# Performance work log

Hardware: AMD Instinct MI355X
Metric: run time of the kernel (lower is better)

## Reference

```python
import jax, jax.numpy as jnp
import numpy as np

B, D, H, W = 8, 256, 128, 128
NCLS, K = 6, 8
RATIO = 0.05
P = int(H * W * RATIO)  # 819 sampled pixels, unique (replace=False in original)


def setup_inputs() -> dict:
    key = jax.random.key(0)
    ks = jax.random.split(key, 6)
    rng = np.random.default_rng(0)
    flat_idx = rng.choice(H * W, P, replace=False)
    return {
        "assp_features": jax.random.normal(ks[0], (B, D, H, W), jnp.float32),
        "prototypes": jax.random.normal(ks[1], (B, NCLS, K, D), jnp.float32),
        "Wk": jax.random.normal(ks[2], (128, D), jnp.float32) * 0.05,
        "bk": jax.random.normal(ks[3], (128,), jnp.float32) * 0.05,
        "Wq": jax.random.normal(ks[4], (NCLS, 128, D), jnp.float32) * 0.05,
        "bq": jax.random.normal(ks[5], (NCLS, 128), jnp.float32) * 0.05,
        "x_coords": jnp.asarray(flat_idx // H, jnp.int32),
        "y_coords": jnp.asarray(flat_idx % H, jnp.int32),
    }


def reference(assp_features, prototypes, Wk, bk, Wq, bq, x_coords, y_coords):
    # DomainTrain branch: detach, then replace sampled pixels with nearest prototype
    feats = jax.lax.stop_gradient(assp_features)                 # [B,D,H,W]
    pf = prototypes.reshape(B, NCLS * K, D)                      # [B,6K,D]
    sel = feats[:, :, x_coords, y_coords].transpose(0, 2, 1)     # [B,P,D]
    # squared distance (||f||^2 constant dropped; argmin unchanged)
    d2 = jnp.sum(pf * pf, -1)[:, None, :] - 2.0 * jnp.einsum('bpd,bcd->bpc', sel, pf)
    idx = jnp.argmin(d2, axis=-1)                                # [B,P]
    newv = jnp.take_along_axis(pf, idx[:, :, None], axis=1)      # [B,P,D]
    feats = feats.at[:, :, x_coords, y_coords].set(newv.transpose(0, 2, 1))

    # key: 1x1 conv -> [B,128,H,W]
    key_out = jnp.einsum('od,bdhw->bohw', Wk, feats) + bk[None, :, None, None]
    # per-class query 1x1 conv applied to each prototype vector -> [B,6,K,128]
    q = jnp.einsum('iod,bijd->bijo', Wq, prototypes) + bq[None, :, None, :]
    # similarity per (class, cluster): [B,6K,H,W], ordering i-major j-minor as in the loop
    sim = jnp.einsum('bijo,bohw->bijhw', q, key_out).reshape(B, NCLS * K, H, W)
    C = NCLS * K
    w = jax.nn.softmax(sim / C * K, axis=1)
    w_max = jnp.max(w, axis=1)                                   # [B,H,W]
    w_mean = jnp.mean(w, axis=1)
    assp_weighted = feats * w_max[:, None]                       # [B,D,H,W]
    prototypes_out = q.reshape(B, NCLS * K, 128).transpose(1, 0, 2)  # list -> stacked [6K,B,128]
    return assp_weighted, prototypes_out, w_max, sim, w_mean
```

## Files before the change

### kernel.cpp

```cpp
#include <hip/hip_runtime.h>

#define B_   8
#define D_   256
#define HW_  16384
#define NC_  48
#define KO_  128
#define PT_  32

using bf16x8 = __attribute__((ext_vector_type(8))) short;
using f32x4  = __attribute__((ext_vector_type(4))) float;
typedef unsigned long long ull;

__device__ __forceinline__ unsigned short f2bf(float f) {
  unsigned int u = __float_as_uint(f);
  u += 0x7FFFu + ((u >> 16) & 1u);
  return (unsigned short)(u >> 16);
}
__device__ __forceinline__ ull pack4bf(float a, float b, float c, float d) {
  return (ull)f2bf(a) | ((ull)f2bf(b) << 16)
       | ((ull)f2bf(c) << 32) | ((ull)f2bf(d) << 48);
}

__global__ __launch_bounds__(128) void p1_kernel(
    const float* __restrict__ protos, const float* __restrict__ Wq,
    const float* __restrict__ bq, const float* __restrict__ Wk,
    const float* __restrict__ bk,
    unsigned short* __restrict__ m_pk, float* __restrict__ beta,
    float* __restrict__ protos_out, int* __restrict__ map_i) {
  __shared__ float qs[KO_];
  const int c = blockIdx.x;
  const int b = blockIdx.y;
  const int o = threadIdx.x;
  const int i = c >> 3;
  const float* wq = Wq + ((size_t)i * KO_ + o) * D_;
  const float* pp = protos + ((size_t)b * NC_ + c) * D_;
  float acc = bq[i * KO_ + o];
  for (int d = 0; d < D_; d += 4) {
    float4 wv = *(const float4*)(wq + d);
    float4 pv = *(const float4*)(pp + d);
    acc += wv.x * pv.x + wv.y * pv.y + wv.z * pv.z + wv.w * pv.w;
  }
  qs[o] = acc;
  protos_out[((size_t)c * B_ + b) * KO_ + o] = acc;
  const int gid = (b * NC_ + c) * KO_ + o;
  if (gid < B_ * HW_ / 4) map_i[gid] = -1;
  __syncthreads();
  float m0 = 0.f, m1 = 0.f;
  for (int oo = 0; oo < KO_; ++oo) {
    float2 wv = *(const float2*)(Wk + (size_t)oo * D_ + o * 2);
    float qv = qs[oo];
    m0 += qv * wv.x;
    m1 += qv * wv.y;
  }
  {
    const int ks = o >> 4, g = (o >> 2) & 3, ii = (o & 3) * 2;
    const int ct = c >> 4, lr = c & 15;
    const size_t fidx = ((size_t)(b * 24 + ks * 3 + ct) * 64 + g * 16 + lr) * 8 + ii;
    unsigned pk = (unsigned)f2bf(m0) | ((unsigned)f2bf(m1) << 16);
    *(unsigned*)(m_pk + fidx) = pk;
  }
  if (o < 64) {
    float p = qs[o] * bk[o] + qs[o + 64] * bk[o + 64];
    for (int off = 32; off; off >>= 1) p += __shfl_down(p, off);
    if (o == 0) beta[b * NC_ + c] = p;
  }
}

__global__ void p2_kernel(const float* __restrict__ feats,
                          const float* __restrict__ protos,
                          const int* __restrict__ xc,
                          const int* __restrict__ yc,
                          signed char* __restrict__ map) {
  const int sp = blockIdx.x;
  const int b  = blockIdx.y;
  const int lane = threadIdx.x;
  __shared__ float sel[D_];
  const int pix = xc[sp] * 128 + yc[sp];
  const float* fb = feats + (size_t)b * D_ * HW_ + pix;
  for (int k = 0; k < 4; ++k) {
    int d = lane + k * 64;
    sel[d] = fb[(size_t)d * HW_];
  }
  __syncthreads();
  float d2 = 3.4e38f;
  int bi = lane;
  if (lane < NC_) {
    const float* pf = protos + ((size_t)b * NC_ + lane) * D_;
    float nrm = 0.f, dot = 0.f;
    for (int d = 0; d < D_; d += 4) {
      float4 pv = *(const float4*)(pf + d);
      float4 sv = *(const float4*)(sel + d);
      nrm += pv.x * pv.x + pv.y * pv.y + pv.z * pv.z + pv.w * pv.w;
      dot += pv.x * sv.x + pv.y * sv.y + pv.z * sv.z + pv.w * sv.w;
    }
    d2 = nrm - 2.f * dot;
  }
  for (int off = 32; off > 0; off >>= 1) {
    float ov = __shfl_down(d2, off);
    int   oi = __shfl_down(bi, off);
    if (ov < d2 || (ov == d2 && oi < bi)) { d2 = ov; bi = oi; }
  }
  if (lane == 0) map[(size_t)b * HW_ + pix] = (signed char)bi;
}

__global__ __launch_bounds__(128, 2) void m_kernel(
    const float* __restrict__ feats, const float* __restrict__ protos,
    const unsigned short* __restrict__ m_pk, const float* __restrict__ beta,
    const signed char* __restrict__ map,
    float* __restrict__ out_assp, float* __restrict__ out_wmax,
    float* __restrict__ out_sim, float* __restrict__ out_wmean) {
  __shared__ __align__(16) unsigned short Fb[PT_ * 256];
  __shared__ __align__(16) float simb[NC_ * PT_];
  __shared__ float wm[PT_];
  __shared__ signed char map_s[PT_];

  const int tid  = threadIdx.x;
  const int lane = tid & 63;
  const int wid  = tid >> 6;
  const int g    = lane >> 4;
  const int lr   = lane & 15;
  const int b    = blockIdx.y;
  const int p0   = blockIdx.x * PT_;

  if (tid < PT_) map_s[tid] = map[(size_t)b * HW_ + p0 + tid];
  __syncthreads();

  unsigned char* fbB = (unsigned char*)Fb;
  const int x  = tid & 7;
  const int dr = tid >> 3;

  float V[64];
  {
    const float* fb = feats + (size_t)b * D_ * HW_ + p0 + x * 4;
    const float* prb = protos + (size_t)b * NC_ * D_;
    int cj[4];
    #pragma unroll
    for (int j = 0; j < 4; ++j) cj[j] = map_s[x * 4 + j];
    #pragma unroll
    for (int it = 0; it < 4; ++it) {
      const int d0 = it * 64 + dr * 4;
      #pragma unroll
      for (int k = 0; k < 4; ++k) {
        float4 t = *(const float4*)(fb + (size_t)(d0 + k) * HW_);
        V[it*16 + k*4 + 0] = t.x; V[it*16 + k*4 + 1] = t.y;
        V[it*16 + k*4 + 2] = t.z; V[it*16 + k*4 + 3] = t.w;
      }
      #pragma unroll
      for (int j = 0; j < 4; ++j) {
        if (cj[j] >= 0) {
          float4 pv = *(const float4*)(prb + (size_t)cj[j] * D_ + d0);
          V[it*16 + 0*4 + j] = pv.x; V[it*16 + 1*4 + j] = pv.y;
          V[it*16 + 2*4 + j] = pv.z; V[it*16 + 3*4 + j] = pv.w;
        }
      }
      #pragma unroll
      for (int j = 0; j < 4; ++j) {
        const int p = x * 4 + j;
        const unsigned X = (unsigned)(((p & 7) << 4) ^ ((p >> 3) << 3));
        *(ull*)(fbB + p * 512 + ((unsigned)(d0 * 2) ^ X)) =
            pack4bf(V[it*16 + 0*4 + j], V[it*16 + 1*4 + j],
                    V[it*16 + 2*4 + j], V[it*16 + 3*4 + j]);
      }
    }
  }
  __syncthreads();

  const int p = wid * 16 + lr;
  const unsigned Xp = (unsigned)(((p & 7) << 4) ^ ((p >> 3) << 3));
  f32x4 sacc[3] = {};
  {
    const unsigned short* apk = m_pk + (size_t)b * 24 * 64 * 8 + lane * 8;
    #pragma unroll
    for (int ks = 0; ks < 8; ++ks) {
      const unsigned base = (unsigned)(ks * 64 + g * 16);
      ull lo = *(const ull*)(fbB + p * 512 + (base ^ Xp));
      ull hi = *(const ull*)(fbB + p * 512 + ((base + 8) ^ Xp));
      union { ull u[2]; bf16x8 v8; } bu;
      bu.u[0] = lo; bu.u[1] = hi;
      #pragma unroll
      for (int ct = 0; ct < 3; ++ct) {
        bf16x8 af = *(const bf16x8*)(apk + (size_t)(ks * 3 + ct) * 64 * 8);
        sacc[ct] = __builtin_amdgcn_mfma_f32_16x16x32_bf16(af, bu.v8, sacc[ct], 0, 0, 0);
      }
    }
  }

  #pragma unroll
  for (int ct = 0; ct < 3; ++ct) {
    float4 bt = *(const float4*)(beta + b * NC_ + ct * 16 + g * 4);
    sacc[ct][0] += bt.x; sacc[ct][1] += bt.y;
    sacc[ct][2] += bt.z; sacc[ct][3] += bt.w;
  }
  float m = -3.4e38f;
  #pragma unroll
  for (int ct = 0; ct < 3; ++ct)
    #pragma unroll
    for (int r = 0; r < 4; ++r) m = fmaxf(m, sacc[ct][r]);
  m = fmaxf(m, __shfl_xor(m, 16));
  m = fmaxf(m, __shfl_xor(m, 32));
  const float sc = 1.0f / 6.0f;
  float s = 0.f;
  #pragma unroll
  for (int ct = 0; ct < 3; ++ct)
    #pragma unroll
    for (int r = 0; r < 4; ++r) s += __expf((sacc[ct][r] - m) * sc);
  s += __shfl_xor(s, 16);
  s += __shfl_xor(s, 32);
  const float wmax = 1.f / s;

  #pragma unroll
  for (int ct = 0; ct < 3; ++ct)
    #pragma unroll
    for (int r = 0; r < 4; ++r)
      simb[(ct * 16 + g * 4 + r) * PT_ + p] = sacc[ct][r];
  const size_t pixg = (size_t)p0 + p;
  if (g == 0) {
    wm[p] = wmax;
    out_wmax[(size_t)b * HW_ + pixg] = wmax;
    out_wmean[(size_t)b * HW_ + pixg] = 1.f / 48.f;
  }
  __syncthreads();

  #pragma unroll
  for (int r3 = 0; r3 < 3; ++r3) {
    const int f  = r3 * 128 + tid;
    const int c  = f >> 3;
    const int po = (f & 7) * 4;
    float4 sv = *(const float4*)(simb + c * PT_ + po);
    *(float4*)(out_sim + ((size_t)b * NC_ + c) * HW_ + p0 + po) = sv;
  }

  {
    float4 w4 = *(const float4*)(wm + x * 4);
    float* oa = out_assp + (size_t)b * D_ * HW_ + p0 + x * 4;
    #pragma unroll
    for (int it = 0; it < 4; ++it) {
      const int d0 = it * 64 + dr * 4;
      #pragma unroll
      for (int k = 0; k < 4; ++k) {
        float4 o;
        o.x = V[it*16 + k*4 + 0] * w4.x;
        o.y = V[it*16 + k*4 + 1] * w4.y;
        o.z = V[it*16 + k*4 + 2] * w4.z;
        o.w = V[it*16 + k*4 + 3] * w4.w;
        *(float4*)(oa + (size_t)(d0 + k) * HW_) = o;
      }
    }
  }
}

extern "C" void kernel_launch(void* const* d_in, const int* in_sizes, int n_in,
                              void* d_out, int out_size, void* d_ws, size_t ws_size,
                              hipStream_t stream) {
  const float* feats  = (const float*)d_in[0];
  const float* protos = (const float*)d_in[1];
  const float* Wk     = (const float*)d_in[2];
  const float* bk     = (const float*)d_in[3];
  const float* Wq     = (const float*)d_in[4];
  const float* bq     = (const float*)d_in[5];
  const int*   xc     = (const int*)d_in[6];
  const int*   yc     = (const int*)d_in[7];
  const int    P      = in_sizes[6];

  float* out       = (float*)d_out;
  float* out_assp  = out;
  float* out_po    = out_assp + (size_t)B_ * D_ * HW_;
  float* out_wmax  = out_po + (size_t)NC_ * B_ * KO_;
  float* out_sim   = out_wmax + (size_t)B_ * HW_;
  float* out_wmean = out_sim + (size_t)B_ * NC_ * HW_;

  unsigned char* ws = (unsigned char*)d_ws;
  unsigned short* m_pk = (unsigned short*)ws;
  float* beta          = (float*)(ws + 196608);
  signed char* map     = (signed char*)(ws + 198144);

  p1_kernel<<<dim3(NC_, B_), 128, 0, stream>>>(protos, Wq, bq, Wk, bk,
                                               m_pk, beta, out_po, (int*)map);
  p2_kernel<<<dim3(P, B_), 64, 0, stream>>>(feats, protos, xc, yc, map);
  m_kernel<<<dim3(HW_ / PT_, B_), 128, 0, stream>>>(feats, protos, m_pk, beta, map,
                                                    out_assp, out_wmax, out_sim, out_wmean);
}
```

Measured before the change: 132.3 us.

## Fuse nearest-prototype search into main kernel and drop separate pixel-map pass

Removes the p2 kernel and its map buffer. The main kernel now builds a per-wave bitmask of sampled pixels from a pixel list prepared in p1, and runs the argmin over prototypes in registers using wave shuffles. p1 is widened to 256 threads, splitting each dot product in half, and also precomputes prototype norms. The sim/assp shared-memory staging and its block barriers are replaced by direct global stores, with the LDS sync reduced to a waitcnt since each wave only reads its own rows. Occupancy hint rises to 3 blocks per CU. Every wave now scans the whole pixel list, and sim stores become narrower and less coalesced.

```diff
diff --git a/kernel.cpp b/kernel.cpp
--- a/kernel.cpp
+++ b/kernel.cpp
@@ -21,149 +21,180 @@
        | ((ull)f2bf(c) << 32) | ((ull)f2bf(d) << 48);
 }
 
-__global__ __launch_bounds__(128) void p1_kernel(
+__global__ __launch_bounds__(256) void p1_kernel(
     const float* __restrict__ protos, const float* __restrict__ Wq,
     const float* __restrict__ bq, const float* __restrict__ Wk,
-    const float* __restrict__ bk,
+    const float* __restrict__ bk, const int* __restrict__ xc,
+    const int* __restrict__ yc,
     unsigned short* __restrict__ m_pk, float* __restrict__ beta,
-    float* __restrict__ protos_out, int* __restrict__ map_i) {
+    float* __restrict__ nrmb, int* __restrict__ pixlist,
+    float* __restrict__ protos_out, int pcnt) {
   __shared__ float qs[KO_];
+  __shared__ float sc2[2][KO_][2];
   const int c = blockIdx.x;
   const int b = blockIdx.y;
-  const int o = threadIdx.x;
+  const int t = threadIdx.x;
+  const int o = t & 127, h = t >> 7;
   const int i = c >> 3;
-  const float* wq = Wq + ((size_t)i * KO_ + o) * D_;
   const float* pp = protos + ((size_t)b * NC_ + c) * D_;
-  float acc = bq[i * KO_ + o];
-  for (int d = 0; d < D_; d += 4) {
-    float4 wv = *(const float4*)(wq + d);
-    float4 pv = *(const float4*)(pp + d);
-    acc += wv.x * pv.x + wv.y * pv.y + wv.z * pv.z + wv.w * pv.w;
-  }
-  qs[o] = acc;
-  protos_out[((size_t)c * B_ + b) * KO_ + o] = acc;
-  const int gid = (b * NC_ + c) * KO_ + o;
-  if (gid < B_ * HW_ / 4) map_i[gid] = -1;
+  {
+    const float* wq = Wq + ((size_t)i * KO_ + o) * D_ + h * 128;
+    const float* ph = pp + h * 128;
+    float acc = 0.f;
+    for (int d = 0; d < 128; d += 4) {
+      float4 wv = *(const float4*)(wq + d);
+      float4 pv = *(const float4*)(ph + d);
+      acc += wv.x * pv.x + wv.y * pv.y + wv.z * pv.z + wv.w * pv.w;
+    }
+    sc2[h][o][0] = acc;
+  }
   __syncthreads();
-  float m0 = 0.f, m1 = 0.f;
-  for (int oo = 0; oo < KO_; ++oo) {
-    float2 wv = *(const float2*)(Wk + (size_t)oo * D_ + o * 2);
-    float qv = qs[oo];
-    m0 += qv * wv.x;
-    m1 += qv * wv.y;
-  }
-  {
-    const int ks = o >> 4, g = (o >> 2) & 3, ii = (o & 3) * 2;
-    const int ct = c >> 4, lr = c & 15;
-    const size_t fidx = ((size_t)(b * 24 + ks * 3 + ct) * 64 + g * 16 + lr) * 8 + ii;
-    unsigned pk = (unsigned)f2bf(m0) | ((unsigned)f2bf(m1) << 16);
-    *(unsigned*)(m_pk + fidx) = pk;
-  }
-  if (o < 64) {
-    float p = qs[o] * bk[o] + qs[o + 64] * bk[o + 64];
-    for (int off = 32; off; off >>= 1) p += __shfl_down(p, off);
-    if (o == 0) beta[b * NC_ + c] = p;
-  }
-}
-
-__global__ void p2_kernel(const float* __restrict__ feats,
-                          const float* __restrict__ protos,
-                          const int* __restrict__ xc,
-                          const int* __restrict__ yc,
-                          signed char* __restrict__ map) {
-  const int sp = blockIdx.x;
-  const int b  = blockIdx.y;
-  const int lane = threadIdx.x;
-  __shared__ float sel[D_];
-  const int pix = xc[sp] * 128 + yc[sp];
-  const float* fb = feats + (size_t)b * D_ * HW_ + pix;
-  for (int k = 0; k < 4; ++k) {
-    int d = lane + k * 64;
-    sel[d] = fb[(size_t)d * HW_];
+  if (h == 0) {
+    float q = sc2[0][o][0] + sc2[1][o][0] + bq[i * KO_ + o];
+    qs[o] = q;
+    protos_out[((size_t)c * B_ + b) * KO_ + o] = q;
   }
   __syncthreads();
-  float d2 = 3.4e38f;
-  int bi = lane;
-  if (lane < NC_) {
-    const float* pf = protos + ((size_t)b * NC_ + lane) * D_;
-    float nrm = 0.f, dot = 0.f;
-    for (int d = 0; d < D_; d += 4) {
-      float4 pv = *(const float4*)(pf + d);
-      float4 sv = *(const float4*)(sel + d);
-      nrm += pv.x * pv.x + pv.y * pv.y + pv.z * pv.z + pv.w * pv.w;
-      dot += pv.x * sv.x + pv.y * sv.y + pv.z * sv.z + pv.w * sv.w;
-    }
-    d2 = nrm - 2.f * dot;
-  }
-  for (int off = 32; off > 0; off >>= 1) {
-    float ov = __shfl_down(d2, off);
-    int   oi = __shfl_down(bi, off);
-    if (ov < d2 || (ov == d2 && oi < bi)) { d2 = ov; bi = oi; }
-  }
-  if (lane == 0) map[(size_t)b * HW_ + pix] = (signed char)bi;
-}
-
-__global__ __launch_bounds__(128, 2) void m_kernel(
+  {
+    float m0 = 0.f, m1 = 0.f;
+    for (int oo = h * 64; oo < h * 64 + 64; ++oo) {
+      float2 wv = *(const float2*)(Wk + (size_t)oo * D_ + o * 2);
+      float qv = qs[oo];
+      m0 += qv * wv.x; m1 += qv * wv.y;
+    }
+    sc2[h][o][0] = m0; sc2[h][o][1] = m1;
+  }
+  __syncthreads();
+  if (h == 0) {
+    float M0 = sc2[0][o][0] + sc2[1][o][0];
+    float M1 = sc2[0][o][1] + sc2[1][o][1];
+    const int ks = o >> 4, gg = (o >> 2) & 3, ii = (o & 3) * 2;
+    const int ct = c >> 4, lrr = c & 15;
+    const size_t fidx = ((size_t)(b * 24 + ks * 3 + ct) * 64 + gg * 16 + lrr) * 8 + ii;
+    *(unsigned*)(m_pk + fidx) = (unsigned)f2bf(M0) | ((unsigned)f2bf(M1) << 16);
+  }
+  if (t < 64) {
+    float p = qs[t] * bk[t] + qs[t + 64] * bk[t + 64];
+    float4 pv = *(const float4*)(pp + t * 4);
+    float nn = pv.x * pv.x + pv.y * pv.y + pv.z * pv.z + pv.w * pv.w;
+    for (int off = 32; off; off >>= 1) {
+      p  += __shfl_down(p, off);
+      nn += __shfl_down(nn, off);
+    }
+    if (t == 0) { beta[b * NC_ + c] = p; nrmb[b * NC_ + c] = nn; }
+  }
+  const int gid = (b * NC_ + c) * 256 + t;
+  if (gid < pcnt) pixlist[gid] = xc[gid] * 128 + yc[gid];
+}
+
+#define EXTRACT_J(J)                                        \
+  _Pragma("unroll")                                         \
+  for (int it = 0; it < 4; ++it) {                          \
+    vsel[it * 4 + 0] = V[it * 16 + 0 * 4 + (J)];            \
+    vsel[it * 4 + 1] = V[it * 16 + 1 * 4 + (J)];            \
+    vsel[it * 4 + 2] = V[it * 16 + 2 * 4 + (J)];            \
+    vsel[it * 4 + 3] = V[it * 16 + 3 * 4 + (J)];            \
+  }
+
+#define SUBST_J(J)                                          \
+  _Pragma("unroll")                                         \
+  for (int it = 0; it < 4; ++it) {                          \
+    float4 pv = *(const float4*)(prc + it * 64);            \
+    V[it * 16 + 0 * 4 + (J)] = pv.x;                        \
+    V[it * 16 + 1 * 4 + (J)] = pv.y;                        \
+    V[it * 16 + 2 * 4 + (J)] = pv.z;                        \
+    V[it * 16 + 3 * 4 + (J)] = pv.w;                        \
+  }
+
+__global__ __launch_bounds__(128, 3) void m_kernel(
     const float* __restrict__ feats, const float* __restrict__ protos,
     const unsigned short* __restrict__ m_pk, const float* __restrict__ beta,
-    const signed char* __restrict__ map,
+    const float* __restrict__ nrmb, const int* __restrict__ pixlist, int pcnt,
     float* __restrict__ out_assp, float* __restrict__ out_wmax,
     float* __restrict__ out_sim, float* __restrict__ out_wmean) {
   __shared__ __align__(16) unsigned short Fb[PT_ * 256];
-  __shared__ __align__(16) float simb[NC_ * PT_];
-  __shared__ float wm[PT_];
-  __shared__ signed char map_s[PT_];
 
   const int tid  = threadIdx.x;
   const int lane = tid & 63;
   const int wid  = tid >> 6;
+  const int pq   = lane & 3;
+  const int dr   = lane >> 2;
   const int g    = lane >> 4;
   const int lr   = lane & 15;
   const int b    = blockIdx.y;
   const int p0   = blockIdx.x * PT_;
-
-  if (tid < PT_) map_s[tid] = map[(size_t)b * HW_ + p0 + tid];
-  __syncthreads();
-
   unsigned char* fbB = (unsigned char*)Fb;
-  const int x  = tid & 7;
-  const int dr = tid >> 3;
 
   float V[64];
-  {
-    const float* fb = feats + (size_t)b * D_ * HW_ + p0 + x * 4;
-    const float* prb = protos + (size_t)b * NC_ * D_;
-    int cj[4];
-    #pragma unroll
-    for (int j = 0; j < 4; ++j) cj[j] = map_s[x * 4 + j];
-    #pragma unroll
-    for (int it = 0; it < 4; ++it) {
-      const int d0 = it * 64 + dr * 4;
+  const float* fb = feats + (size_t)b * D_ * HW_ + p0 + wid * 16 + pq * 4;
+  #pragma unroll
+  for (int it = 0; it < 4; ++it)
+    #pragma unroll
+    for (int k = 0; k < 4; ++k) {
+      float4 t = *(const float4*)(fb + (size_t)(it * 64 + dr * 4 + k) * HW_);
+      V[it*16 + k*4 + 0] = t.x; V[it*16 + k*4 + 1] = t.y;
+      V[it*16 + k*4 + 2] = t.z; V[it*16 + k*4 + 3] = t.w;
+    }
+
+  unsigned lm = 0;
+  {
+    const int wbase = p0 + wid * 16;
+    for (int i2 = lane; i2 < pcnt; i2 += 64) {
+      int dp = pixlist[i2] - wbase;
+      if ((unsigned)dp < 16u) lm |= 1u << dp;
+    }
+    #pragma unroll
+    for (int s = 1; s < 64; s <<= 1) lm |= (unsigned)__shfl_xor((int)lm, s);
+  }
+
+  const float* prb = protos + (size_t)b * NC_ * D_ + dr * 4;
+  while (lm) {
+    const int pp = __ffs(lm) - 1; lm &= lm - 1;
+    const int tq = pp >> 2, j = pp & 3;
+    float vsel[16];
+    switch (j) {
+      case 0: EXTRACT_J(0) break;
+      case 1: EXTRACT_J(1) break;
+      case 2: EXTRACT_J(2) break;
+      default: EXTRACT_J(3) break;
+    }
+    float best = 3.4e38f; int cb = 0;
+    for (int c = 0; c < NC_; ++c) {
+      const float* prc = prb + (size_t)c * D_;
+      float dot = 0.f;
       #pragma unroll
-      for (int k = 0; k < 4; ++k) {
-        float4 t = *(const float4*)(fb + (size_t)(d0 + k) * HW_);
-        V[it*16 + k*4 + 0] = t.x; V[it*16 + k*4 + 1] = t.y;
-        V[it*16 + k*4 + 2] = t.z; V[it*16 + k*4 + 3] = t.w;
+      for (int it = 0; it < 4; ++it) {
+        float4 pv = *(const float4*)(prc + it * 64);
+        dot += pv.x * vsel[it*4+0] + pv.y * vsel[it*4+1]
+             + pv.z * vsel[it*4+2] + pv.w * vsel[it*4+3];
       }
-      #pragma unroll
-      for (int j = 0; j < 4; ++j) {
-        if (cj[j] >= 0) {
-          float4 pv = *(const float4*)(prb + (size_t)cj[j] * D_ + d0);
-          V[it*16 + 0*4 + j] = pv.x; V[it*16 + 1*4 + j] = pv.y;
-          V[it*16 + 2*4 + j] = pv.z; V[it*16 + 3*4 + j] = pv.w;
-        }
+      dot += __shfl_xor(dot, 4);  dot += __shfl_xor(dot, 8);
+      dot += __shfl_xor(dot, 16); dot += __shfl_xor(dot, 32);
+      float d2v = nrmb[b * NC_ + c] - 2.f * dot;
+      if (d2v < best) { best = d2v; cb = c; }
+    }
+    if (pq == tq) {
+      const float* prc = prb + (size_t)cb * D_;
+      switch (j) {
+        case 0: SUBST_J(0) break;
+        case 1: SUBST_J(1) break;
+        case 2: SUBST_J(2) break;
+        default: SUBST_J(3) break;
       }
-      #pragma unroll
-      for (int j = 0; j < 4; ++j) {
-        const int p = x * 4 + j;
-        const unsigned X = (unsigned)(((p & 7) << 4) ^ ((p >> 3) << 3));
-        *(ull*)(fbB + p * 512 + ((unsigned)(d0 * 2) ^ X)) =
-            pack4bf(V[it*16 + 0*4 + j], V[it*16 + 1*4 + j],
-                    V[it*16 + 2*4 + j], V[it*16 + 3*4 + j]);
-      }
-    }
-  }
-  __syncthreads();
+    }
+  }
+
+  #pragma unroll
+  for (int it = 0; it < 4; ++it)
+    #pragma unroll
+    for (int j = 0; j < 4; ++j) {
+      const int p = wid * 16 + pq * 4 + j;
+      const unsigned X = (unsigned)(((p & 7) << 4) ^ ((p >> 3) << 3));
+      *(ull*)(fbB + p * 512 + ((unsigned)(it * 128 + dr * 8) ^ X)) =
+          pack4bf(V[it*16 + 0*4 + j], V[it*16 + 1*4 + j],
+                  V[it*16 + 2*4 + j], V[it*16 + 3*4 + j]);
+    }
+  asm volatile("s_waitcnt lgkmcnt(0)" ::: "memory");
 
   const int p = wid * 16 + lr;
   const unsigned Xp = (unsigned)(((p & 7) << 4) ^ ((p >> 3) << 3));
@@ -208,44 +239,35 @@
   s += __shfl_xor(s, 32);
   const float wmax = 1.f / s;
 
+  const size_t pixg = (size_t)p0 + p;
   #pragma unroll
   for (int ct = 0; ct < 3; ++ct)
     #pragma unroll
     for (int r = 0; r < 4; ++r)
-      simb[(ct * 16 + g * 4 + r) * PT_ + p] = sacc[ct][r];
-  const size_t pixg = (size_t)p0 + p;
+      out_sim[((size_t)b * NC_ + ct * 16 + g * 4 + r) * HW_ + pixg] = sacc[ct][r];
   if (g == 0) {
-    wm[p] = wmax;
     out_wmax[(size_t)b * HW_ + pixg] = wmax;
     out_wmean[(size_t)b * HW_ + pixg] = 1.f / 48.f;
   }
-  __syncthreads();
-
-  #pragma unroll
-  for (int r3 = 0; r3 < 3; ++r3) {
-    const int f  = r3 * 128 + tid;
-    const int c  = f >> 3;
-    const int po = (f & 7) * 4;
-    float4 sv = *(const float4*)(simb + c * PT_ + po);
-    *(float4*)(out_sim + ((size_t)b * NC_ + c) * HW_ + p0 + po) = sv;
-  }
-
-  {
-    float4 w4 = *(const float4*)(wm + x * 4);
-    float* oa = out_assp + (size_t)b * D_ * HW_ + p0 + x * 4;
-    #pragma unroll
-    for (int it = 0; it < 4; ++it) {
-      const int d0 = it * 64 + dr * 4;
+
+  {
+    const float w0 = __shfl(wmax, wid * 64 ? 0 : 0 + pq * 4 + 0);
+    const float w1 = __shfl(wmax, pq * 4 + 1);
+    const float w2 = __shfl(wmax, pq * 4 + 2);
+    const float w3 = __shfl(wmax, pq * 4 + 3);
+    const float ww0 = __shfl(wmax, pq * 4 + 0);
+    float* oa = out_assp + (size_t)b * D_ * HW_ + p0 + wid * 16 + pq * 4;
+    #pragma unroll
+    for (int it = 0; it < 4; ++it)
       #pragma unroll
       for (int k = 0; k < 4; ++k) {
         float4 o;
-        o.x = V[it*16 + k*4 + 0] * w4.x;
-        o.y = V[it*16 + k*4 + 1] * w4.y;
-        o.z = V[it*16 + k*4 + 2] * w4.z;
-        o.w = V[it*16 + k*4 + 3] * w4.w;
-        *(float4*)(oa + (size_t)(d0 + k) * HW_) = o;
+        o.x = V[it*16 + k*4 + 0] * ww0;
+        o.y = V[it*16 + k*4 + 1] * w1;
+        o.z = V[it*16 + k*4 + 2] * w2;
+        o.w = V[it*16 + k*4 + 3] * w3;
+        *(float4*)(oa + (size_t)(it * 64 + dr * 4 + k) * HW_) = o;
       }
-    }
   }
 }
 
@@ -272,11 +294,12 @@
   unsigned char* ws = (unsigned char*)d_ws;
   unsigned short* m_pk = (unsigned short*)ws;
   float* beta          = (float*)(ws + 196608);
-  signed char* map     = (signed char*)(ws + 198144);
-
-  p1_kernel<<<dim3(NC_, B_), 128, 0, stream>>>(protos, Wq, bq, Wk, bk,
-                                               m_pk, beta, out_po, (int*)map);
-  p2_kernel<<<dim3(P, B_), 64, 0, stream>>>(feats, protos, xc, yc, map);
-  m_kernel<<<dim3(HW_ / PT_, B_), 128, 0, stream>>>(feats, protos, m_pk, beta, map,
+  float* nrmb          = (float*)(ws + 198144);
+  int* pixlist         = (int*)(ws + 199680);
+
+  p1_kernel<<<dim3(NC_, B_), 256, 0, stream>>>(protos, Wq, bq, Wk, bk, xc, yc,
+                                               m_pk, beta, nrmb, pixlist, out_po, P);
+  m_kernel<<<dim3(HW_ / PT_, B_), 128, 0, stream>>>(feats, protos, m_pk, beta, nrmb,
+                                                    pixlist, P,
                                                     out_assp, out_wmax, out_sim, out_wmean);
 }
```

Result: slower. 213.0 us (+61.0%).

## Loop main kernel over four pixel tiles with register-resident weight fragments; split p1 reduction

Applied to the files above, without the earlier changes.

The main kernel now handles four 32-pixel tiles per block. It loads the 24 bf16 weight fragments and the bias vectors into registers once and reuses them across all four tiles, instead of reloading them from global memory for every tile. This cuts the grid size by four and amortizes the per-block setup. The cost is higher register pressure, since A adds 96 VGPRs on top of V[64], which may lower occupancy or cause spills, and the tiles within a block run serially with no overlap. Separately, the prototype projection kernel uses 256 threads that each take half of the D and o reductions, then combine the halves through shared memory.

```diff
diff --git a/kernel.cpp b/kernel.cpp
--- a/kernel.cpp
+++ b/kernel.cpp
@@ -6,6 +6,7 @@
 #define NC_  48
 #define KO_  128
 #define PT_  32
+#define TT_  4
 
 using bf16x8 = __attribute__((ext_vector_type(8))) short;
 using f32x4  = __attribute__((ext_vector_type(4))) float;
@@ -21,49 +22,63 @@
        | ((ull)f2bf(c) << 32) | ((ull)f2bf(d) << 48);
 }
 
-__global__ __launch_bounds__(128) void p1_kernel(
+__global__ __launch_bounds__(256) void p1_kernel(
     const float* __restrict__ protos, const float* __restrict__ Wq,
     const float* __restrict__ bq, const float* __restrict__ Wk,
     const float* __restrict__ bk,
     unsigned short* __restrict__ m_pk, float* __restrict__ beta,
     float* __restrict__ protos_out, int* __restrict__ map_i) {
   __shared__ float qs[KO_];
+  __shared__ float sc2[2][KO_][2];
   const int c = blockIdx.x;
   const int b = blockIdx.y;
-  const int o = threadIdx.x;
+  const int t = threadIdx.x;
+  const int o = t & 127, h = t >> 7;
   const int i = c >> 3;
-  const float* wq = Wq + ((size_t)i * KO_ + o) * D_;
   const float* pp = protos + ((size_t)b * NC_ + c) * D_;
-  float acc = bq[i * KO_ + o];
-  for (int d = 0; d < D_; d += 4) {
-    float4 wv = *(const float4*)(wq + d);
-    float4 pv = *(const float4*)(pp + d);
-    acc += wv.x * pv.x + wv.y * pv.y + wv.z * pv.z + wv.w * pv.w;
-  }
-  qs[o] = acc;
-  protos_out[((size_t)c * B_ + b) * KO_ + o] = acc;
-  const int gid = (b * NC_ + c) * KO_ + o;
+  {
+    const float* wq = Wq + ((size_t)i * KO_ + o) * D_ + h * 128;
+    const float* ph = pp + h * 128;
+    float acc = 0.f;
+    for (int d = 0; d < 128; d += 4) {
+      float4 wv = *(const float4*)(wq + d);
+      float4 pv = *(const float4*)(ph + d);
+      acc += wv.x * pv.x + wv.y * pv.y + wv.z * pv.z + wv.w * pv.w;
+    }
+    sc2[h][o][0] = acc;
+  }
+  __syncthreads();
+  if (h == 0) {
+    float q = sc2[0][o][0] + sc2[1][o][0] + bq[i * KO_ + o];
+    qs[o] = q;
+    protos_out[((size_t)c * B_ + b) * KO_ + o] = q;
+  }
+  __syncthreads();
+  {
+    float m0 = 0.f, m1 = 0.f;
+    for (int oo = h * 64; oo < h * 64 + 64; ++oo) {
+      float2 wv = *(const float2*)(Wk + (size_t)oo * D_ + o * 2);
+      float qv = qs[oo];
+      m0 += qv * wv.x; m1 += qv * wv.y;
+    }
+    sc2[h][o][0] = m0; sc2[h][o][1] = m1;
+  }
+  __syncthreads();
+  if (h == 0) {
+    float M0 = sc2[0][o][0] + sc2[1][o][0];
+    float M1 = sc2[0][o][1] + sc2[1][o][1];
+    const int ks = o >> 4, gg = (o >> 2) & 3, ii = (o & 3) * 2;
+    const int ct = c >> 4, lrr = c & 15;
+    const size_t fidx = ((size_t)(b * 24 + ks * 3 + ct) * 64 + gg * 16 + lrr) * 8 + ii;
+    *(unsigned*)(m_pk + fidx) = (unsigned)f2bf(M0) | ((unsigned)f2bf(M1) << 16);
+  }
+  if (t < 64) {
+    float p = qs[t] * bk[t] + qs[t + 64] * bk[t + 64];
+    for (int off = 32; off; off >>= 1) p += __shfl_down(p, off);
+    if (t == 0) beta[b * NC_ + c] = p;
+  }
+  const int gid = (b * NC_ + c) * 256 + t;
   if (gid < B_ * HW_ / 4) map_i[gid] = -1;
-  __syncthreads();
-  float m0 = 0.f, m1 = 0.f;
-  for (int oo = 0; oo < KO_; ++oo) {
-    float2 wv = *(const float2*)(Wk + (size_t)oo * D_ + o * 2);
-    float qv = qs[oo];
-    m0 += qv * wv.x;
-    m1 += qv * wv.y;
-  }
-  {
-    const int ks = o >> 4, g = (o >> 2) & 3, ii = (o & 3) * 2;
-    const int ct = c >> 4, lr = c & 15;
-    const size_t fidx = ((size_t)(b * 24 + ks * 3 + ct) * 64 + g * 16 + lr) * 8 + ii;
-    unsigned pk = (unsigned)f2bf(m0) | ((unsigned)f2bf(m1) << 16);
-    *(unsigned*)(m_pk + fidx) = pk;
-  }
-  if (o < 64) {
-    float p = qs[o] * bk[o] + qs[o + 64] * bk[o + 64];
-    for (int off = 32; off; off >>= 1) p += __shfl_down(p, off);
-    if (o == 0) beta[b * NC_ + c] = p;
-  }
 }
 
 __global__ void p2_kernel(const float* __restrict__ feats,
@@ -112,7 +127,7 @@
   __shared__ __align__(16) unsigned short Fb[PT_ * 256];
   __shared__ __align__(16) float simb[NC_ * PT_];
   __shared__ float wm[PT_];
-  __shared__ signed char map_s[PT_];
+  __shared__ signed char map_s[TT_ * PT_];
 
   const int tid  = threadIdx.x;
   const int lane = tid & 63;
@@ -120,56 +135,69 @@
   const int g    = lane >> 4;
   const int lr   = lane & 15;
   const int b    = blockIdx.y;
-  const int p0   = blockIdx.x * PT_;
-
-  if (tid < PT_) map_s[tid] = map[(size_t)b * HW_ + p0 + tid];
-  __syncthreads();
+  const int P0   = blockIdx.x * (TT_ * PT_);
+
+  map_s[tid] = map[(size_t)b * HW_ + P0 + tid];
+
+  bf16x8 A[24];
+  {
+    const unsigned short* apk = m_pk + (size_t)b * 24 * 64 * 8 + lane * 8;
+    #pragma unroll
+    for (int f = 0; f < 24; ++f)
+      A[f] = *(const bf16x8*)(apk + (size_t)f * 512);
+  }
+  float4 bt[3];
+  #pragma unroll
+  for (int ct = 0; ct < 3; ++ct)
+    bt[ct] = *(const float4*)(beta + b * NC_ + ct * 16 + g * 4);
 
   unsigned char* fbB = (unsigned char*)Fb;
   const int x  = tid & 7;
   const int dr = tid >> 3;
-
-  float V[64];
-  {
-    const float* fb = feats + (size_t)b * D_ * HW_ + p0 + x * 4;
-    const float* prb = protos + (size_t)b * NC_ * D_;
-    int cj[4];
-    #pragma unroll
-    for (int j = 0; j < 4; ++j) cj[j] = map_s[x * 4 + j];
-    #pragma unroll
-    for (int it = 0; it < 4; ++it) {
-      const int d0 = it * 64 + dr * 4;
-      #pragma unroll
-      for (int k = 0; k < 4; ++k) {
-        float4 t = *(const float4*)(fb + (size_t)(d0 + k) * HW_);
-        V[it*16 + k*4 + 0] = t.x; V[it*16 + k*4 + 1] = t.y;
-        V[it*16 + k*4 + 2] = t.z; V[it*16 + k*4 + 3] = t.w;
-      }
-      #pragma unroll
-      for (int j = 0; j < 4; ++j) {
-        if (cj[j] >= 0) {
-          float4 pv = *(const float4*)(prb + (size_t)cj[j] * D_ + d0);
-          V[it*16 + 0*4 + j] = pv.x; V[it*16 + 1*4 + j] = pv.y;
-          V[it*16 + 2*4 + j] = pv.z; V[it*16 + 3*4 + j] = pv.w;
+  const int p  = wid * 16 + lr;
+  const unsigned Xp = (unsigned)(((p & 7) << 4) ^ ((p >> 3) << 3));
+  __syncthreads();
+
+  for (int t = 0; t < TT_; ++t) {
+    const int p0 = P0 + t * PT_;
+
+    float V[64];
+    {
+      const float* fb = feats + (size_t)b * D_ * HW_ + p0 + x * 4;
+      const float* prb = protos + (size_t)b * NC_ * D_;
+      int cj[4];
+      #pragma unroll
+      for (int j = 0; j < 4; ++j) cj[j] = map_s[t * PT_ + x * 4 + j];
+      #pragma unroll
+      for (int it = 0; it < 4; ++it) {
+        const int d0 = it * 64 + dr * 4;
+        #pragma unroll
+        for (int k = 0; k < 4; ++k) {
+          float4 tv = *(const float4*)(fb + (size_t)(d0 + k) * HW_);
+          V[it*16 + k*4 + 0] = tv.x; V[it*16 + k*4 + 1] = tv.y;
+          V[it*16 + k*4 + 2] = tv.z; V[it*16 + k*4 + 3] = tv.w;
+        }
+        #pragma unroll
+        for (int j = 0; j < 4; ++j) {
+          if (cj[j] >= 0) {
+            float4 pv = *(const float4*)(prb + (size_t)cj[j] * D_ + d0);
+            V[it*16 + 0*4 + j] = pv.x; V[it*16 + 1*4 + j] = pv.y;
+            V[it*16 + 2*4 + j] = pv.z; V[it*16 + 3*4 + j] = pv.w;
+          }
+        }
+        #pragma unroll
+        for (int j = 0; j < 4; ++j) {
+          const int pw = x * 4 + j;
+          const unsigned X = (unsigned)(((pw & 7) << 4) ^ ((pw >> 3) << 3));
+          *(ull*)(fbB + pw * 512 + ((unsigned)(d0 * 2) ^ X)) =
+              pack4bf(V[it*16 + 0*4 + j], V[it*16 + 1*4 + j],
+                      V[it*16 + 2*4 + j], V[it*16 + 3*4 + j]);
         }
       }
-      #pragma unroll
-      for (int j = 0; j < 4; ++j) {
-        const int p = x * 4 + j;
-        const unsigned X = (unsigned)(((p & 7) << 4) ^ ((p >> 3) << 3));
-        *(ull*)(fbB + p * 512 + ((unsigned)(d0 * 2) ^ X)) =
-            pack4bf(V[it*16 + 0*4 + j], V[it*16 + 1*4 + j],
-                    V[it*16 + 2*4 + j], V[it*16 + 3*4 + j]);
-      }
-    }
-  }
-  __syncthreads();
-
-  const int p = wid * 16 + lr;
-  const unsigned Xp = (unsigned)(((p & 7) << 4) ^ ((p >> 3) << 3));
-  f32x4 sacc[3] = {};
-  {
-    const unsigned short* apk = m_pk + (size_t)b * 24 * 64 * 8 + lane * 8;
+    }
+    __syncthreads();
+
+    f32x4 sacc[3] = {};
     #pragma unroll
     for (int ks = 0; ks < 8; ++ks) {
       const unsigned base = (unsigned)(ks * 64 + g * 16);
@@ -178,74 +206,73 @@
       union { ull u[2]; bf16x8 v8; } bu;
       bu.u[0] = lo; bu.u[1] = hi;
       #pragma unroll
-      for (int ct = 0; ct < 3; ++ct) {
-        bf16x8 af = *(const bf16x8*)(apk + (size_t)(ks * 3 + ct) * 64 * 8);
-        sacc[ct] = __builtin_amdgcn_mfma_f32_16x16x32_bf16(af, bu.v8, sacc[ct], 0, 0, 0);
+      for (int ct = 0; ct < 3; ++ct)
+        sacc[ct] = __builtin_amdgcn_mfma_f32_16x16x32_bf16(A[ks * 3 + ct], bu.v8,
+                                                           sacc[ct], 0, 0, 0);
+    }
+
+    #pragma unroll
+    for (int ct = 0; ct < 3; ++ct) {
+      sacc[ct][0] += bt[ct].x; sacc[ct][1] += bt[ct].y;
+      sacc[ct][2] += bt[ct].z; sacc[ct][3] += bt[ct].w;
+    }
+    float m = -3.4e38f;
+    #pragma unroll
+    for (int ct = 0; ct < 3; ++ct)
+      #pragma unroll
+      for (int r = 0; r < 4; ++r) m = fmaxf(m, sacc[ct][r]);
+    m = fmaxf(m, __shfl_xor(m, 16));
+    m = fmaxf(m, __shfl_xor(m, 32));
+    const float sc = 1.0f / 6.0f;
+    float s = 0.f;
+    #pragma unroll
+    for (int ct = 0; ct < 3; ++ct)
+      #pragma unroll
+      for (int r = 0; r < 4; ++r) s += __expf((sacc[ct][r] - m) * sc);
+    s += __shfl_xor(s, 16);
+    s += __shfl_xor(s, 32);
+    const float wmax = 1.f / s;
+
+    #pragma unroll
+    for (int ct = 0; ct < 3; ++ct)
+      #pragma unroll
+      for (int r = 0; r < 4; ++r)
+        simb[(ct * 16 + g * 4 + r) * PT_ + p] = sacc[ct][r];
+    const size_t pixg = (size_t)p0 + p;
+    if (g == 0) {
+      wm[p] = wmax;
+      out_wmax[(size_t)b * HW_ + pixg] = wmax;
+      out_wmean[(size_t)b * HW_ + pixg] = 1.f / 48.f;
+    }
+    __syncthreads();
+
+    #pragma unroll
+    for (int r3 = 0; r3 < 3; ++r3) {
+      const int f  = r3 * 128 + tid;
+      const int c  = f >> 3;
+      const int po = (f & 7) * 4;
+      float4 sv = *(const float4*)(simb + c * PT_ + po);
+      *(float4*)(out_sim + ((size_t)b * NC_ + c) * HW_ + p0 + po) = sv;
+    }
+
+    {
+      float4 w4 = *(const float4*)(wm + x * 4);
+      float* oa = out_assp + (size_t)b * D_ * HW_ + p0 + x * 4;
+      #pragma unroll
+      for (int it = 0; it < 4; ++it) {
+        const int d0 = it * 64 + dr * 4;
+        #pragma unroll
+        for (int k = 0; k < 4; ++k) {
+          float4 o;
+          o.x = V[it*16 + k*4 + 0] * w4.x;
+          o.y = V[it*16 + k*4 + 1] * w4.y;
+          o.z = V[it*16 + k*4 + 2] * w4.z;
+          o.w = V[it*16 + k*4 + 3] * w4.w;
+          *(float4*)(oa + (size_t)(d0 + k) * HW_) = o;
+        }
       }
     }
-  }
-
-  #pragma unroll
-  for (int ct = 0; ct < 3; ++ct) {
-    float4 bt = *(const float4*)(beta + b * NC_ + ct * 16 + g * 4);
-    sacc[ct][0] += bt.x; sacc[ct][1] += bt.y;
-    sacc[ct][2] += bt.z; sacc[ct][3] += bt.w;
-  }
-  float m = -3.4e38f;
-  #pragma unroll
-  for (int ct = 0; ct < 3; ++ct)
-    #pragma unroll
-    for (int r = 0; r < 4; ++r) m = fmaxf(m, sacc[ct][r]);
-  m = fmaxf(m, __shfl_xor(m, 16));
-  m = fmaxf(m, __shfl_xor(m, 32));
-  const float sc = 1.0f / 6.0f;
-  float s = 0.f;
-  #pragma unroll
-  for (int ct = 0; ct < 3; ++ct)
-    #pragma unroll
-    for (int r = 0; r < 4; ++r) s += __expf((sacc[ct][r] - m) * sc);
-  s += __shfl_xor(s, 16);
-  s += __shfl_xor(s, 32);
-  const float wmax = 1.f / s;
-
-  #pragma unroll
-  for (int ct = 0; ct < 3; ++ct)
-    #pragma unroll
-    for (int r = 0; r < 4; ++r)
-      simb[(ct * 16 + g * 4 + r) * PT_ + p] = sacc[ct][r];
-  const size_t pixg = (size_t)p0 + p;
-  if (g == 0) {
-    wm[p] = wmax;
-    out_wmax[(size_t)b * HW_ + pixg] = wmax;
-    out_wmean[(size_t)b * HW_ + pixg] = 1.f / 48.f;
-  }
-  __syncthreads();
-
-  #pragma unroll
-  for (int r3 = 0; r3 < 3; ++r3) {
-    const int f  = r3 * 128 + tid;
-    const int c  = f >> 3;
-    const int po = (f & 7) * 4;
-    float4 sv = *(const float4*)(simb + c * PT_ + po);
-    *(float4*)(out_sim + ((size_t)b * NC_ + c) * HW_ + p0 + po) = sv;
-  }
-
-  {
-    float4 w4 = *(const float4*)(wm + x * 4);
-    float* oa = out_assp + (size_t)b * D_ * HW_ + p0 + x * 4;
-    #pragma unroll
-    for (int it = 0; it < 4; ++it) {
-      const int d0 = it * 64 + dr * 4;
-      #pragma unroll
-      for (int k = 0; k < 4; ++k) {
-        float4 o;
-        o.x = V[it*16 + k*4 + 0] * w4.x;
-        o.y = V[it*16 + k*4 + 1] * w4.y;
-        o.z = V[it*16 + k*4 + 2] * w4.z;
-        o.w = V[it*16 + k*4 + 3] * w4.w;
-        *(float4*)(oa + (size_t)(d0 + k) * HW_) = o;
-      }
-    }
+    __syncthreads();
   }
 }
 
@@ -274,9 +301,10 @@
   float* beta          = (float*)(ws + 196608);
   signed char* map     = (signed char*)(ws + 198144);
 
-  p1_kernel<<<dim3(NC_, B_), 128, 0, stream>>>(protos, Wq, bq, Wk, bk,
+  p1_kernel<<<dim3(NC_, B_), 256, 0, stream>>>(protos, Wq, bq, Wk, bk,
                                                m_pk, beta, out_po, (int*)map);
   p2_kernel<<<dim3(P, B_), 64, 0, stream>>>(feats, protos, xc, yc, map);
-  m_kernel<<<dim3(HW_ / PT_, B_), 128, 0, stream>>>(feats, protos, m_pk, beta, map,
-                                                    out_assp, out_wmax, out_sim, out_wmean);
-}
+  m_kernel<<<dim3(HW_ / (TT_ * PT_), B_), 128, 0, stream>>>(feats, protos, m_pk, beta, map,
+                                                            out_assp, out_wmax, out_sim,
+                                                            out_wmean);
+}
```

Result: slower. 143.2 us (+8.2%).
